# Kernel tuning notes

Measured on AMD Instinct MI355X. Metric: run time of the kernel, lower is better.

Reference implementation:

```python
import jax, jax.numpy as jnp
import numpy as np

B, L, D = 4, 2048, 1024
H = 16
HD = D // H  # head_dim = 64
BASE = 10000.0


def rope_cos_sin(seq_len, head_dim, dtype=jnp.float32):
    inv_freq = 1.0 / (BASE ** (jnp.arange(0, head_dim, 2, dtype=jnp.float32) / head_dim))
    t = jnp.arange(seq_len, dtype=jnp.float32)
    freqs = jnp.outer(t, inv_freq)  # [L, HD/2]
    return jnp.cos(freqs).astype(dtype), jnp.sin(freqs).astype(dtype)


def apply_rope(x, cos, sin):
    # x: [B, H, L, HD]; cos/sin: [L, HD/2]
    x1 = x[..., ::2]
    x2 = x[..., 1::2]
    c = cos[None, None, :, :]
    s = sin[None, None, :, :]
    # NOTE: original concatenates halves (does not re-interleave)
    return jnp.concatenate([x1 * c - x2 * s, x1 * s + x2 * c], axis=-1)


def setup_inputs() -> dict:
    key = jax.random.key(0)
    k1, k2, k3 = jax.random.split(key, 3)
    x = jax.random.normal(k1, (B, L, D), dtype=jnp.float32)
    W_qkv = jax.random.normal(k2, (3 * D, D), dtype=jnp.float32) * (D ** -0.5)
    W_proj = jax.random.normal(k3, (D, D), dtype=jnp.float32) * (D ** -0.5)
    return {"x": x, "W_qkv": W_qkv, "W_proj": W_proj}


def reference(x, W_qkv, W_proj):
    b, l, d = x.shape
    scale = HD ** -0.5
    qkv = jnp.einsum('bld,ed->ble', x, W_qkv)            # [B, L, 3D]
    qkv = qkv.reshape(b, l, 3, H, HD)
    q, k, v = (jnp.transpose(qkv[:, :, i], (0, 2, 1, 3)) for i in range(3))  # [B,H,L,HD]
    cos, sin = rope_cos_sin(l, HD, x.dtype)
    q = apply_rope(q, cos, sin)
    k = apply_rope(k, cos, sin)
    attn = jnp.einsum('bhqd,bhkd->bhqk', q, k) * scale   # [B,H,L,L]
    attn = jax.nn.softmax(attn, axis=-1)
    out = jnp.einsum('bhqk,bhkd->bhqd', attn, v)         # [B,H,L,HD]
    out = jnp.transpose(out, (0, 2, 1, 3)).reshape(b, l, d)
    return jnp.einsum('bld,ed->ble', out, W_proj)
```

## Files before the change

kernel.cpp:

```cpp
#include <hip/hip_runtime.h>
#include <hip/hip_bf16.h>

typedef unsigned short u16;
typedef unsigned int u32;
typedef __attribute__((ext_vector_type(8))) short bf16x8;
typedef __attribute__((ext_vector_type(4))) float f32x4;

#define NB 4
#define NL 2048
#define ND 1024
#define NH 16

__device__ __forceinline__ float bf2f(u16 v) {
    union { float f; unsigned u; } x; x.u = ((unsigned)v) << 16; return x.f;
}
__device__ __forceinline__ u16 f2bf(float f) {
    union { __hip_bfloat16 h; u16 u; } x; x.h = __float2bfloat16(f); return x.u;
}
__device__ __forceinline__ u32 pk2(float a, float b) {
    union { float f; u32 u; } x, y; x.f = a; y.f = b;
    return ((x.u + 0x8000u) >> 16) | ((y.u + 0x8000u) & 0xffff0000u);
}
__device__ __forceinline__ u32 pkt(float lo, float hi) {
    union { float f; u32 u; } x, y; x.f = lo; y.f = hi;
    return __builtin_amdgcn_perm(y.u, x.u, 0x07060302u);
}
#if __has_builtin(__builtin_amdgcn_exp2f)
#define EXP2F(x) __builtin_amdgcn_exp2f(x)
#else
#define EXP2F(x) __expf((x) * 0.69314718056f)
#endif

__device__ __forceinline__ void gload_lds16(const u16* g, u16* l) {
    __builtin_amdgcn_global_load_lds(
        (__attribute__((address_space(1))) void*)(g),
        (__attribute__((address_space(3))) void*)(l), 16, 0, 0);
}

__global__ __launch_bounds__(256) void cast_k(const float* __restrict__ in,
                                              u16* __restrict__ out, int n4) {
    int i = blockIdx.x * 256 + threadIdx.x;
    if (i >= n4) return;
    float4 v = *(const float4*)&in[i * 4];
    u16 tmp[4] = {f2bf(v.x), f2bf(v.y), f2bf(v.z), f2bf(v.w)};
    *(ushort4*)&out[i * 4] = *(ushort4*)tmp;
}

__global__ __launch_bounds__(256) void rope_table_k(float* __restrict__ cosT,
                                                    float* __restrict__ sinT) {
    int idx = blockIdx.x * 256 + threadIdx.x;
    int l = idx >> 5, i = idx & 31;
    double invf = pow(10000.0, -((double)(2 * i)) / 64.0);
    double ang = (double)l * invf;
    cosT[idx] = (float)cos(ang);
    sinT[idx] = (float)sin(ang);
}

template <typename OutT>
__global__ __launch_bounds__(256) void gemm_bt(const u16* __restrict__ A,
                                               const u16* __restrict__ Bm,
                                               OutT* __restrict__ C,
                                               int M, int N, int K) {
    __shared__ u16 As[128][64];
    __shared__ u16 Bs[128][64];
    const int t = threadIdx.x;
    const int lane = t & 63, wave = t >> 6;
    const int quad = lane >> 4, lrow = lane & 15;
    const int wr = wave >> 1, wc = wave & 1;
    const size_t m0 = (size_t)blockIdx.y * 128, n0 = (size_t)blockIdx.x * 128;

    const int srow = wave * 32 + (lane >> 3);
    const int scg  = (lane & 7) ^ (lane >> 3);

    f32x4 acc[4][4];
#pragma unroll
    for (int i = 0; i < 4; ++i)
#pragma unroll
        for (int j = 0; j < 4; ++j) acc[i][j] = (f32x4)0.0f;

    for (int k0 = 0; k0 < K; k0 += 64) {
#pragma unroll
        for (int j = 0; j < 4; ++j) {
            gload_lds16(&A[(m0 + srow + j * 8) * K + k0 + scg * 8],
                        &As[wave * 32 + j * 8][0]);
            gload_lds16(&Bm[(n0 + srow + j * 8) * K + k0 + scg * 8],
                        &Bs[wave * 32 + j * 8][0]);
        }
        __syncthreads();
#pragma unroll
        for (int ks = 0; ks < 2; ++ks) {
            bf16x8 av[4], bv[4];
#pragma unroll
            for (int i = 0; i < 4; ++i)
                av[i] = *(const bf16x8*)
                    &As[wr * 64 + i * 16 + lrow][(((ks << 2) | quad) ^ (lrow & 7)) << 3];
#pragma unroll
            for (int j = 0; j < 4; ++j)
                bv[j] = *(const bf16x8*)
                    &Bs[wc * 64 + j * 16 + lrow][(((ks << 2) | quad) ^ (lrow & 7)) << 3];
#pragma unroll
            for (int i = 0; i < 4; ++i)
#pragma unroll
                for (int j = 0; j < 4; ++j)
                    acc[i][j] = __builtin_amdgcn_mfma_f32_16x16x32_bf16(
                        av[i], bv[j], acc[i][j], 0, 0, 0);
        }
        __syncthreads();
    }
#pragma unroll
    for (int i = 0; i < 4; ++i)
#pragma unroll
        for (int r = 0; r < 4; ++r) {
            size_t row = m0 + wr * 64 + i * 16 + quad * 4 + r;
#pragma unroll
            for (int j = 0; j < 4; ++j) {
                size_t col = n0 + wc * 64 + j * 16 + lrow;
                if constexpr (sizeof(OutT) == 4)
                    C[row * N + col] = acc[i][j][r];
                else
                    C[row * N + col] = f2bf(acc[i][j][r]);
            }
        }
}

__global__ __launch_bounds__(256) void rope_qk_k(const u16* __restrict__ qkv,
                                                 const float* __restrict__ cosT,
                                                 const float* __restrict__ sinT,
                                                 u16* __restrict__ Q,
                                                 u16* __restrict__ Ko) {
    const int row = blockIdx.x;
    const int l = row & (NL - 1);
    const int b = row >> 11;
    const int t = threadIdx.x;
    const int h = t >> 4, sub = t & 15;
    const u16* base = qkv + (size_t)row * 3072 + h * 64 + sub * 4;
    uint2 qv = *(const uint2*)base;
    uint2 kv = *(const uint2*)(base + 1024);
    float2 c2 = *(const float2*)&cosT[l * 32 + sub * 2];
    float2 s2 = *(const float2*)&sinT[l * 32 + sub * 2];
    union { float f; u32 u; } w;
    float q0, q1, q2, q3, k0, k1, k2, k3;
    w.u = qv.x << 16; q0 = w.f; w.u = qv.x & 0xffff0000u; q1 = w.f;
    w.u = qv.y << 16; q2 = w.f; w.u = qv.y & 0xffff0000u; q3 = w.f;
    w.u = kv.x << 16; k0 = w.f; w.u = kv.x & 0xffff0000u; k1 = w.f;
    w.u = kv.y << 16; k2 = w.f; w.u = kv.y & 0xffff0000u; k3 = w.f;
    const float SC = 0.180336879f;
    float cq0 = c2.x * SC, sq0 = s2.x * SC, cq1 = c2.y * SC, sq1 = s2.y * SC;
    u32 qlo = pk2(q0 * cq0 - q1 * sq0, q2 * cq1 - q3 * sq1);
    u32 qhi = pk2(q0 * sq0 + q1 * cq0, q2 * sq1 + q3 * cq1);
    u32 klo = pk2(k0 * c2.x - k1 * s2.x, k2 * c2.y - k3 * s2.y);
    u32 khi = pk2(k0 * s2.x + k1 * c2.x, k2 * s2.y + k3 * c2.y);
    size_t ob = ((size_t)(b * NH + h) * NL + l) * 64;
    *(u32*)&Q[ob + sub * 2] = qlo;
    *(u32*)&Q[ob + sub * 2 + 32] = qhi;
    *(u32*)&Ko[ob + sub * 2] = klo;
    *(u32*)&Ko[ob + sub * 2 + 32] = khi;
}

__global__ __launch_bounds__(256) void vt_k(const u16* __restrict__ qkv,
                                            u16* __restrict__ VT) {
    __shared__ u16 tile[64][72];
    const int lt = blockIdx.x;
    const int bh = blockIdx.y;
    const int b = bh >> 4, h = bh & 15;
    const int l0 = lt * 64;
    const int t = threadIdx.x;
#pragma unroll
    for (int c = 0; c < 2; ++c) {
        int flat8 = t * 2 + c;
        int li = flat8 >> 3, dg = flat8 & 7;
        *(uint4*)&tile[li][dg * 8] =
            *(const uint4*)&qkv[((size_t)(b * NL + l0 + li)) * 3072 + 2048 + h * 64 + dg * 8];
    }
    __syncthreads();
#pragma unroll
    for (int c = 0; c < 2; ++c) {
        int flat8 = t * 2 + c;
        int d = flat8 >> 3, lg = flat8 & 7;
        u16 tmp[8];
#pragma unroll
        for (int e = 0; e < 8; ++e) tmp[e] = tile[lg * 8 + e][d];
        *(uint4*)&VT[((size_t)(bh * 64 + d)) * NL + l0 + lg * 8] = *(uint4*)tmp;
    }
}

__global__ __launch_bounds__(512) void attn_k(const u16* __restrict__ Q,
                                              const u16* __restrict__ Kg,
                                              const u16* __restrict__ VT,
                                              u16* __restrict__ Og) {
    __shared__ __align__(16) char smem[51200];
    u16 (*Qs)[64]  = (u16(*)[64])(smem);
    u16 (*Ks)[64]  = (u16(*)[64])(smem + 16384);
    u16 (*VsT)[64] = (u16(*)[64])(smem + 24576);
    const int t = threadIdx.x;
    const int lane = t & 63, wave = t >> 6;
    const int quad = lane >> 4, lq = lane & 15;
    u16 (*Ps)[72] = (u16(*)[72])(smem + 32768 + wave * 2304);

    const int qt = blockIdx.x, bh = blockIdx.y;
    const int q0 = qt * 128;
    const size_t qkbase = (size_t)bh * NL * 64;

    const int rsub = lane >> 3;
    const int scg  = (lane & 7) ^ rsub;

#pragma unroll
    for (int j = 0; j < 2; ++j)
        gload_lds16(&Q[qkbase + (size_t)(q0 + wave * 16 + j * 8 + rsub) * 64 + scg * 8],
                    &Qs[wave * 16 + j * 8][0]);

    const u16* kptr = Kg + qkbase + (size_t)(wave * 8 + rsub) * 64 + scg * 8;
    const u16* vptr = VT + qkbase + (size_t)(wave * 8 + rsub) * NL + scg * 8;

    const bf16x8 ones = (bf16x8)(short)16256;
    f32x4 ot[4];
#pragma unroll
    for (int mt = 0; mt < 4; ++mt) ot[mt] = (f32x4)0.0f;
    f32x4 lacc = (f32x4)0.0f;

    for (int kc = 0; kc < NL / 64; ++kc) {
        __syncthreads();
        gload_lds16(kptr, &Ks[wave * 8][0]);
        gload_lds16(vptr, &VsT[wave * 8][0]);
        kptr += 64 * 64;
        vptr += 64;
        __syncthreads();

        f32x4 st[4];
#pragma unroll
        for (int mt = 0; mt < 4; ++mt) st[mt] = (f32x4)0.0f;
#pragma unroll
        for (int ks = 0; ks < 2; ++ks) {
            bf16x8 bq = *(const bf16x8*)
                &Qs[wave * 16 + lq][(((ks << 2) | quad) ^ (lq & 7)) << 3];
#pragma unroll
            for (int mt = 0; mt < 4; ++mt) {
                bf16x8 ak = *(const bf16x8*)
                    &Ks[mt * 16 + lq][(((ks << 2) | quad) ^ (lq & 7)) << 3];
                st[mt] = __builtin_amdgcn_mfma_f32_16x16x32_bf16(ak, bq, st[mt], 0, 0, 0);
            }
        }

#pragma unroll
        for (int mt = 0; mt < 4; ++mt) {
            *(uint2*)&Ps[lq][mt * 16 + quad * 4] =
                make_uint2(pkt(EXP2F(st[mt][0]), EXP2F(st[mt][1])),
                           pkt(EXP2F(st[mt][2]), EXP2F(st[mt][3])));
        }
        __builtin_amdgcn_s_waitcnt(0xc07f);

#pragma unroll
        for (int ks = 0; ks < 2; ++ks) {
            bf16x8 bp = *(const bf16x8*)&Ps[lq][ks * 32 + quad * 8];
            lacc = __builtin_amdgcn_mfma_f32_16x16x32_bf16(ones, bp, lacc, 0, 0, 0);
#pragma unroll
            for (int mt = 0; mt < 4; ++mt) {
                bf16x8 av = *(const bf16x8*)
                    &VsT[mt * 16 + lq][(((ks << 2) | quad) ^ (lq & 7)) << 3];
                ot[mt] = __builtin_amdgcn_mfma_f32_16x16x32_bf16(av, bp, ot[mt], 0, 0, 0);
            }
        }
    }

    __syncthreads();
    float* OT_ls = (float*)(smem + wave * 4352);
    float* Ls_ls = (float*)(smem + 34816);
#pragma unroll
    for (int mt = 0; mt < 4; ++mt)
#pragma unroll
        for (int r = 0; r < 4; ++r)
            OT_ls[(mt * 16 + quad * 4 + r) * 17 + lq] = ot[mt][r];
    if (quad == 0) Ls_ls[wave * 16 + lq] = lacc[0];
    __builtin_amdgcn_s_waitcnt(0xc07f);

    const int qq = lane >> 2, dblk = lane & 3;
    float rls = 1.0f / Ls_ls[wave * 16 + qq];
    u16 tmp[16];
#pragma unroll
    for (int e = 0; e < 16; ++e)
        tmp[e] = f2bf(OT_ls[(dblk * 16 + e) * 17 + qq] * rls);
    const int b = bh >> 4, h = bh & 15;
    size_t orow = (size_t)b * NL + q0 + wave * 16 + qq;
    size_t obase = orow * 1024 + h * 64 + dblk * 16;
    *(uint4*)&Og[obase] = *(uint4*)&tmp[0];
    *(uint4*)&Og[obase + 8] = *(uint4*)&tmp[8];
}

extern "C" void kernel_launch(void* const* d_in, const int* in_sizes, int n_in,
                              void* d_out, int out_size, void* d_ws, size_t ws_size,
                              hipStream_t stream) {
    const float* x     = (const float*)d_in[0];
    const float* Wqkv  = (const float*)d_in[1];
    const float* Wproj = (const float*)d_in[2];
    float* out = (float*)d_out;

    char* ws = (char*)d_ws;
    u16* qkv     = (u16*)ws;
    u16* attnout = (u16*)ws;
    u16* Qw      = (u16*)(ws + 50331648);
    u16* Kw      = (u16*)(ws + 67108864);
    u16* VTw     = (u16*)(ws + 83886080);
    float* cosT  = (float*)(ws + 100663296);
    float* sinT  = (float*)(ws + 100925440);
    u16* x_bf    = (u16*)(ws + 101187584);
    u16* Wqkv_bf = (u16*)(ws + 117964800);
    u16* Wproj_bf= (u16*)(ws + 124256256);

    rope_table_k<<<256, 256, 0, stream>>>(cosT, sinT);
    cast_k<<<8192, 256, 0, stream>>>(x, x_bf, 2097152);
    cast_k<<<3072, 256, 0, stream>>>(Wqkv, Wqkv_bf, 786432);
    cast_k<<<1024, 256, 0, stream>>>(Wproj, Wproj_bf, 262144);
    gemm_bt<u16><<<dim3(24, 64), 256, 0, stream>>>(x_bf, Wqkv_bf, qkv, 8192, 3072, 1024);
    rope_qk_k<<<8192, 256, 0, stream>>>(qkv, cosT, sinT, Qw, Kw);
    vt_k<<<dim3(32, 64), 256, 0, stream>>>(qkv, VTw);
    attn_k<<<dim3(16, 64), 512, 0, stream>>>(Qw, Kw, VTw, attnout);
    gemm_bt<float><<<dim3(8, 64), 256, 0, stream>>>(attnout, Wproj_bf, out, 8192, 1024, 1024);
}
```

Baseline: 293.6 us.

## Double-buffer K/V in attention, fuse rope with V transpose, merge casts

The attention kernel now double-buffers K and V tiles in LDS, prefetching the next chunk while computing on the current one, which drops one barrier per iteration. Q fragments are hoisted into registers, and the P scratch is XOR-swizzled to reduce bank conflicts. The rope and V-transpose kernels are merged into one pass over qkv, and the three cast kernels become a single launch. The rope table is now computed in single precision, which may differ slightly from the double-precision values used before.

```diff
diff --git a/kernel.cpp b/kernel.cpp
--- a/kernel.cpp
+++ b/kernel.cpp
@@ -6,9 +6,7 @@
 typedef __attribute__((ext_vector_type(8))) short bf16x8;
 typedef __attribute__((ext_vector_type(4))) float f32x4;
 
-#define NB 4
 #define NL 2048
-#define ND 1024
 #define NH 16
 
 __device__ __forceinline__ float bf2f(u16 v) {
@@ -37,23 +35,30 @@
         (__attribute__((address_space(3))) void*)(l), 16, 0, 0);
 }
 
-__global__ __launch_bounds__(256) void cast_k(const float* __restrict__ in,
-                                              u16* __restrict__ out, int n4) {
+__global__ __launch_bounds__(256) void cast_all_k(const float* __restrict__ x,
+                                                  const float* __restrict__ wq,
+                                                  const float* __restrict__ wp,
+                                                  u16* __restrict__ xo,
+                                                  u16* __restrict__ wqo,
+                                                  u16* __restrict__ wpo) {
     int i = blockIdx.x * 256 + threadIdx.x;
-    if (i >= n4) return;
-    float4 v = *(const float4*)&in[i * 4];
+    const float* src; u16* dst; int off;
+    if (i < 2097152)      { src = x;  dst = xo;  off = i; }
+    else if (i < 2883584) { src = wq; dst = wqo; off = i - 2097152; }
+    else                  { src = wp; dst = wpo; off = i - 2883584; }
+    float4 v = *(const float4*)&src[(size_t)off * 4];
     u16 tmp[4] = {f2bf(v.x), f2bf(v.y), f2bf(v.z), f2bf(v.w)};
-    *(ushort4*)&out[i * 4] = *(ushort4*)tmp;
+    *(ushort4*)&dst[(size_t)off * 4] = *(ushort4*)tmp;
 }
 
 __global__ __launch_bounds__(256) void rope_table_k(float* __restrict__ cosT,
                                                     float* __restrict__ sinT) {
     int idx = blockIdx.x * 256 + threadIdx.x;
     int l = idx >> 5, i = idx & 31;
-    double invf = pow(10000.0, -((double)(2 * i)) / 64.0);
-    double ang = (double)l * invf;
-    cosT[idx] = (float)cos(ang);
-    sinT[idx] = (float)sin(ang);
+    float invf = exp2f(-(float)i * 0.41524101186092029f);
+    float ang = (float)l * invf;
+    cosT[idx] = cosf(ang);
+    sinT[idx] = sinf(ang);
 }
 
 template <typename OutT>
@@ -123,79 +128,80 @@
         }
 }
 
-__global__ __launch_bounds__(256) void rope_qk_k(const u16* __restrict__ qkv,
+__global__ __launch_bounds__(256) void rope_vt_k(const u16* __restrict__ qkv,
                                                  const float* __restrict__ cosT,
                                                  const float* __restrict__ sinT,
                                                  u16* __restrict__ Q,
-                                                 u16* __restrict__ Ko) {
-    const int row = blockIdx.x;
-    const int l = row & (NL - 1);
-    const int b = row >> 11;
-    const int t = threadIdx.x;
-    const int h = t >> 4, sub = t & 15;
-    const u16* base = qkv + (size_t)row * 3072 + h * 64 + sub * 4;
-    uint2 qv = *(const uint2*)base;
-    uint2 kv = *(const uint2*)(base + 1024);
-    float2 c2 = *(const float2*)&cosT[l * 32 + sub * 2];
-    float2 s2 = *(const float2*)&sinT[l * 32 + sub * 2];
-    union { float f; u32 u; } w;
-    float q0, q1, q2, q3, k0, k1, k2, k3;
-    w.u = qv.x << 16; q0 = w.f; w.u = qv.x & 0xffff0000u; q1 = w.f;
-    w.u = qv.y << 16; q2 = w.f; w.u = qv.y & 0xffff0000u; q3 = w.f;
-    w.u = kv.x << 16; k0 = w.f; w.u = kv.x & 0xffff0000u; k1 = w.f;
-    w.u = kv.y << 16; k2 = w.f; w.u = kv.y & 0xffff0000u; k3 = w.f;
-    const float SC = 0.180336879f;
-    float cq0 = c2.x * SC, sq0 = s2.x * SC, cq1 = c2.y * SC, sq1 = s2.y * SC;
-    u32 qlo = pk2(q0 * cq0 - q1 * sq0, q2 * cq1 - q3 * sq1);
-    u32 qhi = pk2(q0 * sq0 + q1 * cq0, q2 * sq1 + q3 * cq1);
-    u32 klo = pk2(k0 * c2.x - k1 * s2.x, k2 * c2.y - k3 * s2.y);
-    u32 khi = pk2(k0 * s2.x + k1 * c2.x, k2 * s2.y + k3 * c2.y);
-    size_t ob = ((size_t)(b * NH + h) * NL + l) * 64;
-    *(u32*)&Q[ob + sub * 2] = qlo;
-    *(u32*)&Q[ob + sub * 2 + 32] = qhi;
-    *(u32*)&Ko[ob + sub * 2] = klo;
-    *(u32*)&Ko[ob + sub * 2 + 32] = khi;
-}
-
-__global__ __launch_bounds__(256) void vt_k(const u16* __restrict__ qkv,
-                                            u16* __restrict__ VT) {
-    __shared__ u16 tile[64][72];
-    const int lt = blockIdx.x;
-    const int bh = blockIdx.y;
+                                                 u16* __restrict__ Ko,
+                                                 u16* __restrict__ VT) {
+    __shared__ u16 vtile[64][72];
+    const int lt = blockIdx.x, bh = blockIdx.y;
     const int b = bh >> 4, h = bh & 15;
     const int l0 = lt * 64;
     const int t = threadIdx.x;
+    const float SC = 0.180336879f;
 #pragma unroll
     for (int c = 0; c < 2; ++c) {
-        int flat8 = t * 2 + c;
+        int flat8 = c * 256 + t;
         int li = flat8 >> 3, dg = flat8 & 7;
-        *(uint4*)&tile[li][dg * 8] =
-            *(const uint4*)&qkv[((size_t)(b * NL + l0 + li)) * 3072 + 2048 + h * 64 + dg * 8];
+        const u16* rowp = qkv + (size_t)(b * NL + l0 + li) * 3072 + h * 64 + dg * 8;
+        uint4 qv = *(const uint4*)rowp;
+        uint4 kv = *(const uint4*)(rowp + 1024);
+        uint4 vv = *(const uint4*)(rowp + 2048);
+        *(uint4*)&vtile[li][dg * 8] = vv;
+        float4 cs = *(const float4*)&cosT[(l0 + li) * 32 + dg * 4];
+        float4 sn = *(const float4*)&sinT[(l0 + li) * 32 + dg * 4];
+        union { float f; u32 u; } w;
+        float e0, o0, e1, o1, e2, o2, e3, o3;
+        w.u = qv.x << 16; e0 = w.f; w.u = qv.x & 0xffff0000u; o0 = w.f;
+        w.u = qv.y << 16; e1 = w.f; w.u = qv.y & 0xffff0000u; o1 = w.f;
+        w.u = qv.z << 16; e2 = w.f; w.u = qv.z & 0xffff0000u; o2 = w.f;
+        w.u = qv.w << 16; e3 = w.f; w.u = qv.w & 0xffff0000u; o3 = w.f;
+        float c0 = cs.x * SC, c1 = cs.y * SC, c2 = cs.z * SC, c3 = cs.w * SC;
+        float s0 = sn.x * SC, s1 = sn.y * SC, s2 = sn.z * SC, s3 = sn.w * SC;
+        size_t ob = ((size_t)(b * NH + h) * NL + l0 + li) * 64;
+        *(uint2*)&Q[ob + dg * 4] =
+            make_uint2(pk2(e0 * c0 - o0 * s0, e1 * c1 - o1 * s1),
+                       pk2(e2 * c2 - o2 * s2, e3 * c3 - o3 * s3));
+        *(uint2*)&Q[ob + 32 + dg * 4] =
+            make_uint2(pk2(e0 * s0 + o0 * c0, e1 * s1 + o1 * c1),
+                       pk2(e2 * s2 + o2 * c2, e3 * s3 + o3 * c3));
+        float f0, g0, f1, g1, f2, g2, f3, g3;
+        w.u = kv.x << 16; f0 = w.f; w.u = kv.x & 0xffff0000u; g0 = w.f;
+        w.u = kv.y << 16; f1 = w.f; w.u = kv.y & 0xffff0000u; g1 = w.f;
+        w.u = kv.z << 16; f2 = w.f; w.u = kv.z & 0xffff0000u; g2 = w.f;
+        w.u = kv.w << 16; f3 = w.f; w.u = kv.w & 0xffff0000u; g3 = w.f;
+        *(uint2*)&Ko[ob + dg * 4] =
+            make_uint2(pk2(f0 * cs.x - g0 * sn.x, f1 * cs.y - g1 * sn.y),
+                       pk2(f2 * cs.z - g2 * sn.z, f3 * cs.w - g3 * sn.w));
+        *(uint2*)&Ko[ob + 32 + dg * 4] =
+            make_uint2(pk2(f0 * sn.x + g0 * cs.x, f1 * sn.y + g1 * cs.y),
+                       pk2(f2 * sn.z + g2 * cs.z, f3 * sn.w + g3 * cs.w));
     }
     __syncthreads();
 #pragma unroll
     for (int c = 0; c < 2; ++c) {
-        int flat8 = t * 2 + c;
+        int flat8 = c * 256 + t;
         int d = flat8 >> 3, lg = flat8 & 7;
         u16 tmp[8];
 #pragma unroll
-        for (int e = 0; e < 8; ++e) tmp[e] = tile[lg * 8 + e][d];
+        for (int e = 0; e < 8; ++e) tmp[e] = vtile[lg * 8 + e][d];
         *(uint4*)&VT[((size_t)(bh * 64 + d)) * NL + l0 + lg * 8] = *(uint4*)tmp;
     }
 }
 
-__global__ __launch_bounds__(512) void attn_k(const u16* __restrict__ Q,
-                                              const u16* __restrict__ Kg,
-                                              const u16* __restrict__ VT,
-                                              u16* __restrict__ Og) {
-    __shared__ __align__(16) char smem[51200];
-    u16 (*Qs)[64]  = (u16(*)[64])(smem);
-    u16 (*Ks)[64]  = (u16(*)[64])(smem + 16384);
-    u16 (*VsT)[64] = (u16(*)[64])(smem + 24576);
+__global__ __launch_bounds__(512, 6) void attn_k(const u16* __restrict__ Q,
+                                                 const u16* __restrict__ Kg,
+                                                 const u16* __restrict__ VT,
+                                                 u16* __restrict__ Og) {
+    __shared__ __align__(16) char smem[49152];
+    u16 (*KsB)[64][64] = (u16(*)[64][64])(smem);
+    u16 (*VsB)[64][64] = (u16(*)[64][64])(smem + 16384);
+    u16* PsBase = (u16*)(smem + 32768);
     const int t = threadIdx.x;
     const int lane = t & 63, wave = t >> 6;
     const int quad = lane >> 4, lq = lane & 15;
-    u16 (*Ps)[72] = (u16(*)[72])(smem + 32768 + wave * 2304);
+    u16* PsW = PsBase + wave * 1024;
 
     const int qt = blockIdx.x, bh = blockIdx.y;
     const int q0 = qt * 128;
@@ -204,13 +210,22 @@
     const int rsub = lane >> 3;
     const int scg  = (lane & 7) ^ rsub;
 
+    u16 (*Qtmp)[64] = (u16(*)[64])(smem + 32768);
 #pragma unroll
     for (int j = 0; j < 2; ++j)
         gload_lds16(&Q[qkbase + (size_t)(q0 + wave * 16 + j * 8 + rsub) * 64 + scg * 8],
-                    &Qs[wave * 16 + j * 8][0]);
-
+                    &Qtmp[wave * 16 + j * 8][0]);
     const u16* kptr = Kg + qkbase + (size_t)(wave * 8 + rsub) * 64 + scg * 8;
     const u16* vptr = VT + qkbase + (size_t)(wave * 8 + rsub) * NL + scg * 8;
+    gload_lds16(kptr, &KsB[0][wave * 8][0]);
+    gload_lds16(vptr, &VsB[0][wave * 8][0]);
+    kptr += 64 * 64;
+    vptr += 64;
+    __syncthreads();
+    bf16x8 bq[2];
+#pragma unroll
+    for (int ks = 0; ks < 2; ++ks)
+        bq[ks] = *(const bf16x8*)&Qtmp[wave * 16 + lq][(((ks << 2) | quad) ^ (lq & 7)) << 3];
 
     const bf16x8 ones = (bf16x8)(short)16256;
     f32x4 ot[4];
@@ -220,30 +235,30 @@
 
     for (int kc = 0; kc < NL / 64; ++kc) {
         __syncthreads();
-        gload_lds16(kptr, &Ks[wave * 8][0]);
-        gload_lds16(vptr, &VsT[wave * 8][0]);
-        kptr += 64 * 64;
-        vptr += 64;
-        __syncthreads();
+        if (kc < NL / 64 - 1) {
+            gload_lds16(kptr, &KsB[(kc + 1) & 1][wave * 8][0]);
+            gload_lds16(vptr, &VsB[(kc + 1) & 1][wave * 8][0]);
+            kptr += 64 * 64;
+            vptr += 64;
+        }
+        const int cur = kc & 1;
 
         f32x4 st[4];
 #pragma unroll
         for (int mt = 0; mt < 4; ++mt) st[mt] = (f32x4)0.0f;
 #pragma unroll
-        for (int ks = 0; ks < 2; ++ks) {
-            bf16x8 bq = *(const bf16x8*)
-                &Qs[wave * 16 + lq][(((ks << 2) | quad) ^ (lq & 7)) << 3];
+        for (int ks = 0; ks < 2; ++ks)
 #pragma unroll
             for (int mt = 0; mt < 4; ++mt) {
                 bf16x8 ak = *(const bf16x8*)
-                    &Ks[mt * 16 + lq][(((ks << 2) | quad) ^ (lq & 7)) << 3];
-                st[mt] = __builtin_amdgcn_mfma_f32_16x16x32_bf16(ak, bq, st[mt], 0, 0, 0);
+                    &KsB[cur][mt * 16 + lq][(((ks << 2) | quad) ^ (lq & 7)) << 3];
+                st[mt] = __builtin_amdgcn_mfma_f32_16x16x32_bf16(ak, bq[ks], st[mt], 0, 0, 0);
             }
-        }
 
 #pragma unroll
         for (int mt = 0; mt < 4; ++mt) {
-            *(uint2*)&Ps[lq][mt * 16 + quad * 4] =
+            int pblk = (mt * 2 + (quad >> 1)) ^ (lq & 7);
+            *(uint2*)&PsW[lq * 64 + pblk * 8 + (quad & 1) * 4] =
                 make_uint2(pkt(EXP2F(st[mt][0]), EXP2F(st[mt][1])),
                            pkt(EXP2F(st[mt][2]), EXP2F(st[mt][3])));
         }
@@ -251,12 +266,13 @@
 
 #pragma unroll
         for (int ks = 0; ks < 2; ++ks) {
-            bf16x8 bp = *(const bf16x8*)&Ps[lq][ks * 32 + quad * 8];
+            bf16x8 bp = *(const bf16x8*)
+                &PsW[lq * 64 + ((((ks << 2) | quad)) ^ (lq & 7)) * 8];
             lacc = __builtin_amdgcn_mfma_f32_16x16x32_bf16(ones, bp, lacc, 0, 0, 0);
 #pragma unroll
             for (int mt = 0; mt < 4; ++mt) {
                 bf16x8 av = *(const bf16x8*)
-                    &VsT[mt * 16 + lq][(((ks << 2) | quad) ^ (lq & 7)) << 3];
+                    &VsB[cur][mt * 16 + lq][(((ks << 2) | quad) ^ (lq & 7)) << 3];
                 ot[mt] = __builtin_amdgcn_mfma_f32_16x16x32_bf16(av, bp, ot[mt], 0, 0, 0);
             }
         }
@@ -307,12 +323,9 @@
     u16* Wproj_bf= (u16*)(ws + 124256256);
 
     rope_table_k<<<256, 256, 0, stream>>>(cosT, sinT);
-    cast_k<<<8192, 256, 0, stream>>>(x, x_bf, 2097152);
-    cast_k<<<3072, 256, 0, stream>>>(Wqkv, Wqkv_bf, 786432);
-    cast_k<<<1024, 256, 0, stream>>>(Wproj, Wproj_bf, 262144);
+    cast_all_k<<<12288, 256, 0, stream>>>(x, Wqkv, Wproj, x_bf, Wqkv_bf, Wproj_bf);
     gemm_bt<u16><<<dim3(24, 64), 256, 0, stream>>>(x_bf, Wqkv_bf, qkv, 8192, 3072, 1024);
-    rope_qk_k<<<8192, 256, 0, stream>>>(qkv, cosT, sinT, Qw, Kw);
-    vt_k<<<dim3(32, 64), 256, 0, stream>>>(qkv, VTw);
+    rope_vt_k<<<dim3(32, 64), 256, 0, stream>>>(qkv, cosT, sinT, Qw, Kw, VTw);
     attn_k<<<dim3(16, 64), 512, 0, stream>>>(Qw, Kw, VTw, attnout);
     gemm_bt<float><<<dim3(8, 64), 256, 0, stream>>>(attnout, Wproj_bf, out, 8192, 1024, 1024);
 }
```

New measurement: 280.1 us. -4.6%, faster.
